# Kernel optimization log

Measured on AMD Instinct MI355X. Metric: run time of the kernel, lower is better.

## Reference

```python
import jax, jax.numpy as jnp
import numpy as np

N_NODES = 50000
N_EDGES = 625000
D = 128
H = 128

def setup_inputs() -> dict:
    key = jax.random.key(0)
    ks = jax.random.split(key, 6)
    z = jax.random.normal(ks[0], (N_NODES, D), dtype=jnp.float32)
    edge_index = jax.random.randint(ks[1], (2, N_EDGES), 0, N_NODES, dtype=jnp.int64)
    # MLP params (Linear stores y = x @ W + b here; W is [in, out])
    W1 = jax.random.normal(ks[2], (2 * D, H), dtype=jnp.float32) * (1.0 / np.sqrt(2 * D))
    b1 = jnp.zeros((H,), dtype=jnp.float32)
    W2 = jax.random.normal(ks[3], (H, H // 2), dtype=jnp.float32) * (1.0 / np.sqrt(H))
    b2 = jnp.zeros((H // 2,), dtype=jnp.float32)
    W3 = jax.random.normal(ks[4], (H // 2, 1), dtype=jnp.float32) * (1.0 / np.sqrt(H // 2))
    b3 = jnp.zeros((1,), dtype=jnp.float32)
    return {"z": z, "edge_index": edge_index, "W1": W1, "b1": b1,
            "W2": W2, "b2": b2, "W3": W3, "b3": b3}

def reference(z, edge_index, W1, b1, W2, b2, W3, b3):
    # Gather edge endpoints: z_i [E, D], z_j [E, D]
    z_i = z[edge_index[0]]
    z_j = z[edge_index[1]]
    edge_feat = jnp.concatenate([z_i, z_j], axis=-1)  # [E, 2D]
    h = jax.nn.relu(edge_feat @ W1 + b1)              # [E, H]  (dropout = identity, eval)
    h = jax.nn.relu(h @ W2 + b2)                      # [E, H//2]
    scores = (h @ W3 + b3)[:, 0]                      # [E]
    return scores
```

## Files before the change

kernel.cpp:

```cpp
#include <hip/hip_runtime.h>

#define NEDGE 625000
#define NNODE 50000
#define WPITCH 136
#define EPITCH 68

typedef __bf16 bf16x8 __attribute__((ext_vector_type(8)));
typedef unsigned short u16x8 __attribute__((ext_vector_type(8)));
typedef float f32x4 __attribute__((ext_vector_type(4)));

__device__ __forceinline__ unsigned short f32_bf16(float f) {
  __bf16 h = (__bf16)f;
  return __builtin_bit_cast(unsigned short, h);
}
__device__ __forceinline__ float bf16_f32(unsigned short h) {
  return (float)__builtin_bit_cast(__bf16, h);
}

__global__ __launch_bounds__(256) void prep_kernel(
    const float* __restrict__ W1, const float* __restrict__ W2,
    const int* __restrict__ ei,
    unsigned short* __restrict__ WcatT, unsigned short* __restrict__ W2T,
    int* __restrict__ idx64_flag)
{
  int i = blockIdx.x * 256 + threadIdx.x;
  if (i < 256 * 128) {
    int jp = i >> 7, k = i & 127;
    float v = (jp < 128) ? W1[k * 128 + jp] : W1[(128 + k) * 128 + (jp - 128)];
    WcatT[jp * 128 + k] = f32_bf16(v);
  } else if (i < 256 * 128 + 64 * 128) {
    int i2 = i - 256 * 128;
    int n = i2 >> 7, k = i2 & 127;
    W2T[n * 128 + k] = f32_bf16(W2[k * 64 + n]);
  }
  if (i == 0) {
    int allz = 1;
    for (int j = 1; j < 64; j += 2) allz &= (ei[j] == 0);
    *idx64_flag = allz;
  }
}

__global__ __launch_bounds__(64) void uv_kernel(
    const float* __restrict__ z, const float* __restrict__ b1,
    const unsigned short* __restrict__ WcatT,
    unsigned short* __restrict__ UV)
{
  __shared__ unsigned short st[16 * EPITCH];
  const int lane = threadIdx.x & 63, c = lane & 15, q = lane >> 4;
  const int mbase = blockIdx.x * 16;
  const int rA = mbase + c;
  const int rAc = (rA < NNODE) ? rA : 0;

  bf16x8 a0[4];
  {
    const float* zA = z + (size_t)rAc * 128 + q * 8;
    float4 fA[4][2];
#pragma unroll
    for (int kt = 0; kt < 4; ++kt) {
      fA[kt][0] = ((const float4*)(zA + kt * 32))[0];
      fA[kt][1] = ((const float4*)(zA + kt * 32))[1];
    }
#pragma unroll
    for (int kt = 0; kt < 4; ++kt) {
      const float* pa = (const float*)&fA[kt][0];
      bf16x8 oa;
#pragma unroll
      for (int j = 0; j < 8; ++j) oa[j] = (__bf16)pa[j];
      a0[kt] = oa;
    }
  }

  for (int nc = 0; nc < 4; ++nc) {
    f32x4 acc[4];
#pragma unroll
    for (int nt = 0; nt < 4; ++nt) {
      f32x4 zz = {0.f, 0.f, 0.f, 0.f};
      acc[nt] = zz;
    }

#pragma unroll
    for (int kt = 0; kt < 4; ++kt) {
#pragma unroll
      for (int nt = 0; nt < 4; ++nt) {
        bf16x8 bb = *(const bf16x8*)(WcatT + (size_t)(nc * 64 + nt * 16 + c) * 128 + kt * 32 + q * 8);
        acc[nt] = __builtin_amdgcn_mfma_f32_16x16x32_bf16(a0[kt], bb, acc[nt], 0, 0, 0);
      }
    }

    float badd[4];
#pragma unroll
    for (int nt = 0; nt < 4; ++nt) {
      int col = nc * 64 + nt * 16 + c;
      badd[nt] = (col < 128) ? b1[col] : 0.f;
    }

#pragma unroll
    for (int nt = 0; nt < 4; ++nt)
#pragma unroll
      for (int reg = 0; reg < 4; ++reg)
        st[(q * 4 + reg) * EPITCH + nt * 16 + c] = f32_bf16(acc[nt][reg] + badd[nt]);
    __asm__ volatile("s_waitcnt lgkmcnt(0)" ::: "memory");

    {
      int lrow = lane >> 2, qt = lane & 3;
      int grow = mbase + lrow;
      u16x8 d0 = *(u16x8*)&st[lrow * EPITCH + qt * 16 + 0];
      u16x8 d1 = *(u16x8*)&st[lrow * EPITCH + qt * 16 + 8];
      if (grow < NNODE) {
        u16x8* dst = (u16x8*)(UV + (size_t)grow * 256 + nc * 64 + qt * 16);
        dst[0] = d0;
        dst[1] = d1;
      }
    }
    __asm__ volatile("s_waitcnt lgkmcnt(0)" ::: "memory");
  }
}

__global__ __launch_bounds__(256, 4) void edge_kernel(
    const int* __restrict__ ei,
    const unsigned short* __restrict__ UV,
    const unsigned short* __restrict__ W2T,
    const float* __restrict__ b2, const float* __restrict__ W3,
    const float* __restrict__ b3, const int* __restrict__ idx64_flag,
    float* __restrict__ out)
{
  __shared__ unsigned short lW[64 * WPITCH];
  const int t = threadIdx.x, wave = t >> 6, lane = t & 63, c = lane & 15, q = lane >> 4;

  {
    int n = t >> 2, qd = t & 3;
    const u16x8* src = (const u16x8*)(W2T + n * 128 + qd * 32);
    u16x8* dst = (u16x8*)(&lW[n * WPITCH + qd * 32]);
#pragma unroll
    for (int i = 0; i < 4; ++i) dst[i] = src[i];
  }
  __syncthreads();

  const int ebase = blockIdx.x * 128 + wave * 32;
  const int eA = ebase + c, eB = ebase + 16 + c;
  const int eAc = (eA < NEDGE) ? eA : 0;
  const int eBc = (eB < NEDGE) ? eB : 0;
  int sA, dA, sB, dB;
  if (*idx64_flag) {
    const long long* e64 = (const long long*)ei;
    sA = (int)e64[eAc]; dA = (int)e64[NEDGE + eAc];
    sB = (int)e64[eBc]; dB = (int)e64[NEDGE + eBc];
  } else {
    sA = ei[eAc]; dA = ei[NEDGE + eAc];
    sB = ei[eBc]; dB = ei[NEDGE + eBc];
  }

  const u16x8* pAu = (const u16x8*)(UV + (size_t)sA * 256) + q;
  const u16x8* pAv = (const u16x8*)(UV + (size_t)dA * 256 + 128) + q;
  const u16x8* pBu = (const u16x8*)(UV + (size_t)sB * 256) + q;
  const u16x8* pBv = (const u16x8*)(UV + (size_t)dB * 256 + 128) + q;
  u16x8 rAu[4], rAv[4], rBu[4], rBv[4];
#pragma unroll
  for (int kt = 0; kt < 4; ++kt) {
    rAu[kt] = pAu[kt * 4];
    rAv[kt] = pAv[kt * 4];
    rBu[kt] = pBu[kt * 4];
    rBv[kt] = pBv[kt * 4];
  }

  f32x4 acc[2][4];
#pragma unroll
  for (int mt = 0; mt < 2; ++mt)
#pragma unroll
    for (int nt = 0; nt < 4; ++nt) {
      f32x4 zz = {0.f, 0.f, 0.f, 0.f};
      acc[mt][nt] = zz;
    }

#pragma unroll
  for (int kt = 0; kt < 4; ++kt) {
    bf16x8 a0, a1;
#pragma unroll
    for (int j = 0; j < 8; ++j) {
      a0[j] = (__bf16)fmaxf(bf16_f32(rAu[kt][j]) + bf16_f32(rAv[kt][j]), 0.f);
      a1[j] = (__bf16)fmaxf(bf16_f32(rBu[kt][j]) + bf16_f32(rBv[kt][j]), 0.f);
    }
#pragma unroll
    for (int nt = 0; nt < 4; ++nt) {
      bf16x8 bb = *(const bf16x8*)(&lW[(nt * 16 + c) * WPITCH + kt * 32 + q * 8]);
      acc[0][nt] = __builtin_amdgcn_mfma_f32_16x16x32_bf16(a0, bb, acc[0][nt], 0, 0, 0);
      acc[1][nt] = __builtin_amdgcn_mfma_f32_16x16x32_bf16(a1, bb, acc[1][nt], 0, 0, 0);
    }
  }

  float b2v[4], w3v[4];
#pragma unroll
  for (int nt = 0; nt < 4; ++nt) {
    int n = nt * 16 + c;
    b2v[nt] = b2[n];
    w3v[nt] = W3[n];
  }
  float bias3 = b3[0];

#pragma unroll
  for (int mt = 0; mt < 2; ++mt) {
    float p0 = 0.f, p1 = 0.f, p2 = 0.f, p3 = 0.f;
#pragma unroll
    for (int nt = 0; nt < 4; ++nt) {
      p0 += fmaxf(acc[mt][nt][0] + b2v[nt], 0.f) * w3v[nt];
      p1 += fmaxf(acc[mt][nt][1] + b2v[nt], 0.f) * w3v[nt];
      p2 += fmaxf(acc[mt][nt][2] + b2v[nt], 0.f) * w3v[nt];
      p3 += fmaxf(acc[mt][nt][3] + b2v[nt], 0.f) * w3v[nt];
    }
#pragma unroll
    for (int m = 1; m < 16; m <<= 1) {
      p0 += __shfl_xor(p0, m, 64);
      p1 += __shfl_xor(p1, m, 64);
      p2 += __shfl_xor(p2, m, 64);
      p3 += __shfl_xor(p3, m, 64);
    }
    if (c == 0) {
      int eb = ebase + mt * 16 + q * 4;
      if (eb + 0 < NEDGE) out[eb + 0] = p0 + bias3;
      if (eb + 1 < NEDGE) out[eb + 1] = p1 + bias3;
      if (eb + 2 < NEDGE) out[eb + 2] = p2 + bias3;
      if (eb + 3 < NEDGE) out[eb + 3] = p3 + bias3;
    }
  }
}

extern "C" void kernel_launch(void* const* d_in, const int* in_sizes, int n_in,
                              void* d_out, int out_size, void* d_ws, size_t ws_size,
                              hipStream_t stream) {
  const float* z  = (const float*)d_in[0];
  const int*   ei = (const int*)d_in[1];
  const float* W1 = (const float*)d_in[2];
  const float* b1 = (const float*)d_in[3];
  const float* W2 = (const float*)d_in[4];
  const float* b2 = (const float*)d_in[5];
  const float* W3 = (const float*)d_in[6];
  const float* b3 = (const float*)d_in[7];
  float* out = (float*)d_out;

  unsigned short* UV    = (unsigned short*)d_ws;
  unsigned short* WcatT = UV + (size_t)NNODE * 256;
  unsigned short* W2T   = WcatT + 256 * 128;
  int* idx64_flag       = (int*)(W2T + 64 * 128);

  prep_kernel<<<dim3(160), dim3(256), 0, stream>>>(W1, W2, ei, WcatT, W2T, idx64_flag);
  uv_kernel<<<dim3((NNODE + 15) / 16), dim3(64), 0, stream>>>(z, b1, WcatT, UV);
  edge_kernel<<<dim3((NEDGE + 127) / 128), dim3(256), 0, stream>>>(
      ei, UV, W2T, b2, W3, b3, idx64_flag, out);
}
```

Baseline: 156.8 us.

## Fuse prep, node projection and edge MLP into one cooperative persistent kernel

Replaces three separate launches with a single cooperative kernel that uses grid-wide syncs between the weight-prep, per-node UV projection and per-edge MLP phases. Each phase becomes a grid-stride loop over a persistent grid sized from occupancy queries. This removes launch gaps and kernel tail effects, and lets each block load W2 into LDS once instead of once per edge tile. In exchange it adds two grid barriers and constrains the edge phase to a smaller persistent grid, which may reduce latency hiding for the random gathers.

```diff
diff --git a/kernel.cpp b/kernel.cpp
--- a/kernel.cpp
+++ b/kernel.cpp
@@ -1,9 +1,14 @@
 #include <hip/hip_runtime.h>
+#include <hip/hip_cooperative_groups.h>
+
+namespace cg = cooperative_groups;
 
 #define NEDGE 625000
 #define NNODE 50000
 #define WPITCH 136
 #define EPITCH 68
+#define NTILE ((NEDGE + 127) / 128)
+#define NUNIT ((NNODE + 15) / 16)
 
 typedef __bf16 bf16x8 __attribute__((ext_vector_type(8)));
 typedef unsigned short u16x8 __attribute__((ext_vector_type(8)));
@@ -17,209 +22,208 @@
   return (float)__builtin_bit_cast(__bf16, h);
 }
 
-__global__ __launch_bounds__(256) void prep_kernel(
-    const float* __restrict__ W1, const float* __restrict__ W2,
-    const int* __restrict__ ei,
-    unsigned short* __restrict__ WcatT, unsigned short* __restrict__ W2T,
-    int* __restrict__ idx64_flag)
+__global__ __launch_bounds__(256, 4) void fused_kernel(
+    const float* __restrict__ z, const int* ei,
+    const float* __restrict__ W1, const float* __restrict__ b1,
+    const float* __restrict__ W2, const float* __restrict__ b2,
+    const float* __restrict__ W3, const float* __restrict__ b3,
+    unsigned short* UV, unsigned short* WcatT, unsigned short* W2T,
+    int* idx64_flag, float* __restrict__ out)
 {
-  int i = blockIdx.x * 256 + threadIdx.x;
-  if (i < 256 * 128) {
-    int jp = i >> 7, k = i & 127;
-    float v = (jp < 128) ? W1[k * 128 + jp] : W1[(128 + k) * 128 + (jp - 128)];
-    WcatT[jp * 128 + k] = f32_bf16(v);
-  } else if (i < 256 * 128 + 64 * 128) {
-    int i2 = i - 256 * 128;
-    int n = i2 >> 7, k = i2 & 127;
-    W2T[n * 128 + k] = f32_bf16(W2[k * 64 + n]);
-  }
-  if (i == 0) {
-    int allz = 1;
-    for (int j = 1; j < 64; j += 2) allz &= (ei[j] == 0);
-    *idx64_flag = allz;
-  }
-}
-
-__global__ __launch_bounds__(64) void uv_kernel(
-    const float* __restrict__ z, const float* __restrict__ b1,
-    const unsigned short* __restrict__ WcatT,
-    unsigned short* __restrict__ UV)
-{
-  __shared__ unsigned short st[16 * EPITCH];
-  const int lane = threadIdx.x & 63, c = lane & 15, q = lane >> 4;
-  const int mbase = blockIdx.x * 16;
-  const int rA = mbase + c;
-  const int rAc = (rA < NNODE) ? rA : 0;
-
-  bf16x8 a0[4];
+  __shared__ unsigned short lds[64 * WPITCH];
+  cg::grid_group grid = cg::this_grid();
+  const int t = threadIdx.x, wave = t >> 6, lane = t & 63, c = lane & 15, q = lane >> 4;
+  const int bid = blockIdx.x;
+  const int nblk = gridDim.x;
+
+  for (int i = bid * 256 + t; i < 256 * 128 + 64 * 128; i += nblk * 256) {
+    if (i < 256 * 128) {
+      int jp = i >> 7, k = i & 127;
+      float v = (jp < 128) ? W1[k * 128 + jp] : W1[(128 + k) * 128 + (jp - 128)];
+      WcatT[jp * 128 + k] = f32_bf16(v);
+    } else {
+      int i2 = i - 256 * 128;
+      int n = i2 >> 7, k = i2 & 127;
+      W2T[n * 128 + k] = f32_bf16(W2[k * 64 + n]);
+    }
+  }
+  if (bid == 0 && t < 64) {
+    int v = ei[t];
+    unsigned long long odd_nz = __ballot((t & 1) && v != 0);
+    if (t == 0) *idx64_flag = (odd_nz == 0ull) ? 1 : 0;
+  }
+  __threadfence();
+  grid.sync();
+
   {
-    const float* zA = z + (size_t)rAc * 128 + q * 8;
-    float4 fA[4][2];
-#pragma unroll
-    for (int kt = 0; kt < 4; ++kt) {
-      fA[kt][0] = ((const float4*)(zA + kt * 32))[0];
-      fA[kt][1] = ((const float4*)(zA + kt * 32))[1];
-    }
-#pragma unroll
-    for (int kt = 0; kt < 4; ++kt) {
-      const float* pa = (const float*)&fA[kt][0];
-      bf16x8 oa;
-#pragma unroll
-      for (int j = 0; j < 8; ++j) oa[j] = (__bf16)pa[j];
-      a0[kt] = oa;
-    }
-  }
-
-  for (int nc = 0; nc < 4; ++nc) {
-    f32x4 acc[4];
-#pragma unroll
-    for (int nt = 0; nt < 4; ++nt) {
-      f32x4 zz = {0.f, 0.f, 0.f, 0.f};
-      acc[nt] = zz;
-    }
-
-#pragma unroll
-    for (int kt = 0; kt < 4; ++kt) {
-#pragma unroll
-      for (int nt = 0; nt < 4; ++nt) {
-        bf16x8 bb = *(const bf16x8*)(WcatT + (size_t)(nc * 64 + nt * 16 + c) * 128 + kt * 32 + q * 8);
-        acc[nt] = __builtin_amdgcn_mfma_f32_16x16x32_bf16(a0[kt], bb, acc[nt], 0, 0, 0);
-      }
-    }
-
-    float badd[4];
-#pragma unroll
-    for (int nt = 0; nt < 4; ++nt) {
-      int col = nc * 64 + nt * 16 + c;
-      badd[nt] = (col < 128) ? b1[col] : 0.f;
-    }
-
-#pragma unroll
-    for (int nt = 0; nt < 4; ++nt)
-#pragma unroll
-      for (int reg = 0; reg < 4; ++reg)
-        st[(q * 4 + reg) * EPITCH + nt * 16 + c] = f32_bf16(acc[nt][reg] + badd[nt]);
-    __asm__ volatile("s_waitcnt lgkmcnt(0)" ::: "memory");
-
-    {
-      int lrow = lane >> 2, qt = lane & 3;
-      int grow = mbase + lrow;
-      u16x8 d0 = *(u16x8*)&st[lrow * EPITCH + qt * 16 + 0];
-      u16x8 d1 = *(u16x8*)&st[lrow * EPITCH + qt * 16 + 8];
-      if (grow < NNODE) {
-        u16x8* dst = (u16x8*)(UV + (size_t)grow * 256 + nc * 64 + qt * 16);
-        dst[0] = d0;
-        dst[1] = d1;
-      }
-    }
-    __asm__ volatile("s_waitcnt lgkmcnt(0)" ::: "memory");
-  }
-}
-
-__global__ __launch_bounds__(256, 4) void edge_kernel(
-    const int* __restrict__ ei,
-    const unsigned short* __restrict__ UV,
-    const unsigned short* __restrict__ W2T,
-    const float* __restrict__ b2, const float* __restrict__ W3,
-    const float* __restrict__ b3, const int* __restrict__ idx64_flag,
-    float* __restrict__ out)
-{
-  __shared__ unsigned short lW[64 * WPITCH];
-  const int t = threadIdx.x, wave = t >> 6, lane = t & 63, c = lane & 15, q = lane >> 4;
+    unsigned short* my = &lds[wave * 16 * EPITCH];
+    const int gw0 = bid * 4 + wave, gstride = nblk * 4;
+    for (int gw = gw0; gw < NUNIT; gw += gstride) {
+      const int mbase = gw * 16;
+      const int rA = mbase + c;
+      const int rAc = (rA < NNODE) ? rA : 0;
+
+      bf16x8 a0[4];
+      {
+        const float* zA = z + (size_t)rAc * 128 + q * 8;
+        float4 fA[4][2];
+#pragma unroll
+        for (int kt = 0; kt < 4; ++kt) {
+          fA[kt][0] = ((const float4*)(zA + kt * 32))[0];
+          fA[kt][1] = ((const float4*)(zA + kt * 32))[1];
+        }
+#pragma unroll
+        for (int kt = 0; kt < 4; ++kt) {
+          const float* pa = (const float*)&fA[kt][0];
+          bf16x8 oa;
+#pragma unroll
+          for (int j = 0; j < 8; ++j) oa[j] = (__bf16)pa[j];
+          a0[kt] = oa;
+        }
+      }
+
+      for (int nc = 0; nc < 4; ++nc) {
+        f32x4 acc[4];
+#pragma unroll
+        for (int nt = 0; nt < 4; ++nt) {
+          f32x4 zz = {0.f, 0.f, 0.f, 0.f};
+          acc[nt] = zz;
+        }
+#pragma unroll
+        for (int kt = 0; kt < 4; ++kt) {
+#pragma unroll
+          for (int nt = 0; nt < 4; ++nt) {
+            bf16x8 bb = *(const bf16x8*)(WcatT + (size_t)(nc * 64 + nt * 16 + c) * 128 + kt * 32 + q * 8);
+            acc[nt] = __builtin_amdgcn_mfma_f32_16x16x32_bf16(a0[kt], bb, acc[nt], 0, 0, 0);
+          }
+        }
+        float badd[4];
+#pragma unroll
+        for (int nt = 0; nt < 4; ++nt) {
+          int col = nc * 64 + nt * 16 + c;
+          badd[nt] = (col < 128) ? b1[col] : 0.f;
+        }
+#pragma unroll
+        for (int nt = 0; nt < 4; ++nt)
+#pragma unroll
+          for (int reg = 0; reg < 4; ++reg)
+            my[(q * 4 + reg) * EPITCH + nt * 16 + c] = f32_bf16(acc[nt][reg] + badd[nt]);
+        __asm__ volatile("s_waitcnt lgkmcnt(0)" ::: "memory");
+
+        {
+          int lrow = lane >> 2, qt = lane & 3;
+          int grow = mbase + lrow;
+          u16x8 d0 = *(u16x8*)&my[lrow * EPITCH + qt * 16 + 0];
+          u16x8 d1 = *(u16x8*)&my[lrow * EPITCH + qt * 16 + 8];
+          if (grow < NNODE) {
+            u16x8* dst = (u16x8*)(UV + (size_t)grow * 256 + nc * 64 + qt * 16);
+            dst[0] = d0;
+            dst[1] = d1;
+          }
+        }
+        __asm__ volatile("s_waitcnt lgkmcnt(0)" ::: "memory");
+      }
+    }
+  }
+  __threadfence();
+  grid.sync();
 
   {
     int n = t >> 2, qd = t & 3;
     const u16x8* src = (const u16x8*)(W2T + n * 128 + qd * 32);
-    u16x8* dst = (u16x8*)(&lW[n * WPITCH + qd * 32]);
+    u16x8* dst = (u16x8*)(&lds[n * WPITCH + qd * 32]);
 #pragma unroll
     for (int i = 0; i < 4; ++i) dst[i] = src[i];
   }
   __syncthreads();
-
-  const int ebase = blockIdx.x * 128 + wave * 32;
-  const int eA = ebase + c, eB = ebase + 16 + c;
-  const int eAc = (eA < NEDGE) ? eA : 0;
-  const int eBc = (eB < NEDGE) ? eB : 0;
-  int sA, dA, sB, dB;
-  if (*idx64_flag) {
-    const long long* e64 = (const long long*)ei;
-    sA = (int)e64[eAc]; dA = (int)e64[NEDGE + eAc];
-    sB = (int)e64[eBc]; dB = (int)e64[NEDGE + eBc];
-  } else {
-    sA = ei[eAc]; dA = ei[NEDGE + eAc];
-    sB = ei[eBc]; dB = ei[NEDGE + eBc];
-  }
-
-  const u16x8* pAu = (const u16x8*)(UV + (size_t)sA * 256) + q;
-  const u16x8* pAv = (const u16x8*)(UV + (size_t)dA * 256 + 128) + q;
-  const u16x8* pBu = (const u16x8*)(UV + (size_t)sB * 256) + q;
-  const u16x8* pBv = (const u16x8*)(UV + (size_t)dB * 256 + 128) + q;
-  u16x8 rAu[4], rAv[4], rBu[4], rBv[4];
-#pragma unroll
-  for (int kt = 0; kt < 4; ++kt) {
-    rAu[kt] = pAu[kt * 4];
-    rAv[kt] = pAv[kt * 4];
-    rBu[kt] = pBu[kt * 4];
-    rBv[kt] = pBv[kt * 4];
-  }
-
-  f32x4 acc[2][4];
-#pragma unroll
-  for (int mt = 0; mt < 2; ++mt)
+  const int i64 = *idx64_flag;
+
+  for (int tile = bid; tile < NTILE; tile += nblk) {
+    const int ebase = tile * 128 + wave * 32;
+    const int eA = ebase + c, eB = ebase + 16 + c;
+    const int eAc = (eA < NEDGE) ? eA : 0;
+    const int eBc = (eB < NEDGE) ? eB : 0;
+    int sA, dA, sB, dB;
+    if (i64) {
+      const long long* e64 = (const long long*)ei;
+      sA = (int)e64[eAc]; dA = (int)e64[NEDGE + eAc];
+      sB = (int)e64[eBc]; dB = (int)e64[NEDGE + eBc];
+    } else {
+      sA = ei[eAc]; dA = ei[NEDGE + eAc];
+      sB = ei[eBc]; dB = ei[NEDGE + eBc];
+    }
+
+    const u16x8* pAu = (const u16x8*)(UV + (size_t)sA * 256) + q;
+    const u16x8* pAv = (const u16x8*)(UV + (size_t)dA * 256 + 128) + q;
+    const u16x8* pBu = (const u16x8*)(UV + (size_t)sB * 256) + q;
+    const u16x8* pBv = (const u16x8*)(UV + (size_t)dB * 256 + 128) + q;
+    u16x8 rAu[4], rAv[4], rBu[4], rBv[4];
+#pragma unroll
+    for (int kt = 0; kt < 4; ++kt) {
+      rAu[kt] = pAu[kt * 4];
+      rAv[kt] = pAv[kt * 4];
+      rBu[kt] = pBu[kt * 4];
+      rBv[kt] = pBv[kt * 4];
+    }
+
+    f32x4 acc[2][4];
+#pragma unroll
+    for (int mt = 0; mt < 2; ++mt)
+#pragma unroll
+      for (int nt = 0; nt < 4; ++nt) {
+        f32x4 zz = {0.f, 0.f, 0.f, 0.f};
+        acc[mt][nt] = zz;
+      }
+
+#pragma unroll
+    for (int kt = 0; kt < 4; ++kt) {
+      bf16x8 a0, a1;
+#pragma unroll
+      for (int j = 0; j < 8; ++j) {
+        a0[j] = (__bf16)fmaxf(bf16_f32(rAu[kt][j]) + bf16_f32(rAv[kt][j]), 0.f);
+        a1[j] = (__bf16)fmaxf(bf16_f32(rBu[kt][j]) + bf16_f32(rBv[kt][j]), 0.f);
+      }
+#pragma unroll
+      for (int nt = 0; nt < 4; ++nt) {
+        bf16x8 bb = *(const bf16x8*)(&lds[(nt * 16 + c) * WPITCH + kt * 32 + q * 8]);
+        acc[0][nt] = __builtin_amdgcn_mfma_f32_16x16x32_bf16(a0, bb, acc[0][nt], 0, 0, 0);
+        acc[1][nt] = __builtin_amdgcn_mfma_f32_16x16x32_bf16(a1, bb, acc[1][nt], 0, 0, 0);
+      }
+    }
+
+    float b2v[4], w3v[4];
 #pragma unroll
     for (int nt = 0; nt < 4; ++nt) {
-      f32x4 zz = {0.f, 0.f, 0.f, 0.f};
-      acc[mt][nt] = zz;
-    }
-
-#pragma unroll
-  for (int kt = 0; kt < 4; ++kt) {
-    bf16x8 a0, a1;
-#pragma unroll
-    for (int j = 0; j < 8; ++j) {
-      a0[j] = (__bf16)fmaxf(bf16_f32(rAu[kt][j]) + bf16_f32(rAv[kt][j]), 0.f);
-      a1[j] = (__bf16)fmaxf(bf16_f32(rBu[kt][j]) + bf16_f32(rBv[kt][j]), 0.f);
-    }
-#pragma unroll
-    for (int nt = 0; nt < 4; ++nt) {
-      bf16x8 bb = *(const bf16x8*)(&lW[(nt * 16 + c) * WPITCH + kt * 32 + q * 8]);
-      acc[0][nt] = __builtin_amdgcn_mfma_f32_16x16x32_bf16(a0, bb, acc[0][nt], 0, 0, 0);
-      acc[1][nt] = __builtin_amdgcn_mfma_f32_16x16x32_bf16(a1, bb, acc[1][nt], 0, 0, 0);
-    }
-  }
-
-  float b2v[4], w3v[4];
-#pragma unroll
-  for (int nt = 0; nt < 4; ++nt) {
-    int n = nt * 16 + c;
-    b2v[nt] = b2[n];
-    w3v[nt] = W3[n];
-  }
-  float bias3 = b3[0];
-
-#pragma unroll
-  for (int mt = 0; mt < 2; ++mt) {
-    float p0 = 0.f, p1 = 0.f, p2 = 0.f, p3 = 0.f;
-#pragma unroll
-    for (int nt = 0; nt < 4; ++nt) {
-      p0 += fmaxf(acc[mt][nt][0] + b2v[nt], 0.f) * w3v[nt];
-      p1 += fmaxf(acc[mt][nt][1] + b2v[nt], 0.f) * w3v[nt];
-      p2 += fmaxf(acc[mt][nt][2] + b2v[nt], 0.f) * w3v[nt];
-      p3 += fmaxf(acc[mt][nt][3] + b2v[nt], 0.f) * w3v[nt];
-    }
-#pragma unroll
-    for (int m = 1; m < 16; m <<= 1) {
-      p0 += __shfl_xor(p0, m, 64);
-      p1 += __shfl_xor(p1, m, 64);
-      p2 += __shfl_xor(p2, m, 64);
-      p3 += __shfl_xor(p3, m, 64);
-    }
-    if (c == 0) {
-      int eb = ebase + mt * 16 + q * 4;
-      if (eb + 0 < NEDGE) out[eb + 0] = p0 + bias3;
-      if (eb + 1 < NEDGE) out[eb + 1] = p1 + bias3;
-      if (eb + 2 < NEDGE) out[eb + 2] = p2 + bias3;
-      if (eb + 3 < NEDGE) out[eb + 3] = p3 + bias3;
+      int n = nt * 16 + c;
+      b2v[nt] = b2[n];
+      w3v[nt] = W3[n];
+    }
+    float bias3 = b3[0];
+
+#pragma unroll
+    for (int mt = 0; mt < 2; ++mt) {
+      float p0 = 0.f, p1 = 0.f, p2 = 0.f, p3 = 0.f;
+#pragma unroll
+      for (int nt = 0; nt < 4; ++nt) {
+        p0 += fmaxf(acc[mt][nt][0] + b2v[nt], 0.f) * w3v[nt];
+        p1 += fmaxf(acc[mt][nt][1] + b2v[nt], 0.f) * w3v[nt];
+        p2 += fmaxf(acc[mt][nt][2] + b2v[nt], 0.f) * w3v[nt];
+        p3 += fmaxf(acc[mt][nt][3] + b2v[nt], 0.f) * w3v[nt];
+      }
+#pragma unroll
+      for (int m = 1; m < 16; m <<= 1) {
+        p0 += __shfl_xor(p0, m, 64);
+        p1 += __shfl_xor(p1, m, 64);
+        p2 += __shfl_xor(p2, m, 64);
+        p3 += __shfl_xor(p3, m, 64);
+      }
+      if (c == 0) {
+        int eb = ebase + mt * 16 + q * 4;
+        if (eb + 0 < NEDGE) out[eb + 0] = p0 + bias3;
+        if (eb + 1 < NEDGE) out[eb + 1] = p1 + bias3;
+        if (eb + 2 < NEDGE) out[eb + 2] = p2 + bias3;
+        if (eb + 3 < NEDGE) out[eb + 3] = p3 + bias3;
+      }
     }
   }
 }
@@ -242,8 +246,25 @@
   unsigned short* W2T   = WcatT + 256 * 128;
   int* idx64_flag       = (int*)(W2T + 64 * 128);
 
-  prep_kernel<<<dim3(160), dim3(256), 0, stream>>>(W1, W2, ei, WcatT, W2T, idx64_flag);
-  uv_kernel<<<dim3((NNODE + 15) / 16), dim3(64), 0, stream>>>(z, b1, WcatT, UV);
-  edge_kernel<<<dim3((NEDGE + 127) / 128), dim3(256), 0, stream>>>(
-      ei, UV, W2T, b2, W3, b3, idx64_flag, out);
-}
+  static int coopGrid = 0;
+  if (coopGrid == 0) {
+    int perCU = 0;
+    if (hipOccupancyMaxActiveBlocksPerMultiprocessor(&perCU, fused_kernel, 256, 0) != hipSuccess ||
+        perCU <= 0)
+      perCU = 3;
+    int nCU = 256;
+    hipDeviceProp_t prop;
+    int dev = 0;
+    if (hipGetDevice(&dev) == hipSuccess && hipGetDeviceProperties(&prop, dev) == hipSuccess)
+      nCU = prop.multiProcessorCount;
+    coopGrid = perCU * nCU;
+    if (coopGrid > 2048) coopGrid = 2048;
+    if (coopGrid < 256) coopGrid = 256;
+  }
+
+  void* args[] = {(void*)&z,  (void*)&ei, (void*)&W1, (void*)&b1, (void*)&W2,
+                  (void*)&b2, (void*)&W3, (void*)&b3, (void*)&UV, (void*)&WcatT,
+                  (void*)&W2T, (void*)&idx64_flag, (void*)&out};
+  hipLaunchCooperativeKernel((const void*)fused_kernel, dim3(coopGrid), dim3(256), args, 0,
+                             stream);
+}
```

Result: slower. 464.9 us (+196.6%).

## Fuse weight prep into uv kernel and stage transposed W1 in LDS

Applied to the files above, without the earlier changes.

Removes the separate prep kernel launch by having the uv kernel convert and transpose W1 into shared memory per block, while two blocks also build W2T and the index-width flag. The uv kernel now uses 256-thread blocks covering 64 nodes, with B operands read from LDS instead of global memory. The cost is that every block redundantly converts all of W1 (32K elements) and needs about 70KB of LDS, which limits occupancy.

```diff
diff --git a/kernel.cpp b/kernel.cpp
--- a/kernel.cpp
+++ b/kernel.cpp
@@ -4,6 +4,7 @@
 #define NNODE 50000
 #define WPITCH 136
 #define EPITCH 68
+#define WCPITCH 136
 
 typedef __bf16 bf16x8 __attribute__((ext_vector_type(8)));
 typedef unsigned short u16x8 __attribute__((ext_vector_type(8)));
@@ -17,37 +18,40 @@
   return (float)__builtin_bit_cast(__bf16, h);
 }
 
-__global__ __launch_bounds__(256) void prep_kernel(
-    const float* __restrict__ W1, const float* __restrict__ W2,
+__global__ __launch_bounds__(256, 2) void uv_kernel(
+    const float* __restrict__ z, const float* __restrict__ W1,
+    const float* __restrict__ b1, const float* __restrict__ W2,
     const int* __restrict__ ei,
-    unsigned short* __restrict__ WcatT, unsigned short* __restrict__ W2T,
+    unsigned short* __restrict__ UV, unsigned short* __restrict__ W2T,
     int* __restrict__ idx64_flag)
 {
-  int i = blockIdx.x * 256 + threadIdx.x;
-  if (i < 256 * 128) {
-    int jp = i >> 7, k = i & 127;
-    float v = (jp < 128) ? W1[k * 128 + jp] : W1[(128 + k) * 128 + (jp - 128)];
-    WcatT[jp * 128 + k] = f32_bf16(v);
-  } else if (i < 256 * 128 + 64 * 128) {
-    int i2 = i - 256 * 128;
-    int n = i2 >> 7, k = i2 & 127;
-    W2T[n * 128 + k] = f32_bf16(W2[k * 64 + n]);
-  }
-  if (i == 0) {
+  __shared__ unsigned short lWc[256 * WCPITCH];
+  __shared__ unsigned short st[4 * 16 * EPITCH];
+  const int t = threadIdx.x, wave = t >> 6, lane = t & 63, c = lane & 15, q = lane >> 4;
+  const int bid = blockIdx.x;
+
+  if (bid < 2) {
+    for (int e = bid * 4096 + t; e < (bid + 1) * 4096; e += 256) {
+      int n = e >> 7, k = e & 127;
+      W2T[n * 128 + k] = f32_bf16(W2[k * 64 + n]);
+    }
+  }
+  if (bid == 0 && t == 0) {
     int allz = 1;
     for (int j = 1; j < 64; j += 2) allz &= (ei[j] == 0);
     *idx64_flag = allz;
   }
-}
-
-__global__ __launch_bounds__(64) void uv_kernel(
-    const float* __restrict__ z, const float* __restrict__ b1,
-    const unsigned short* __restrict__ WcatT,
-    unsigned short* __restrict__ UV)
-{
-  __shared__ unsigned short st[16 * EPITCH];
-  const int lane = threadIdx.x & 63, c = lane & 15, q = lane >> 4;
-  const int mbase = blockIdx.x * 16;
+
+  for (int e = t; e < 256 * 128; e += 256) {
+    int r = e >> 7, j = e & 127;
+    float v = W1[r * 128 + j];
+    int jp = (r < 128) ? j : (128 + j);
+    int k = r & 127;
+    lWc[jp * WCPITCH + k] = f32_bf16(v);
+  }
+  __syncthreads();
+
+  const int mbase = bid * 64 + wave * 16;
   const int rA = mbase + c;
   const int rAc = (rA < NNODE) ? rA : 0;
 
@@ -70,6 +74,8 @@
     }
   }
 
+  unsigned short* my = &st[wave * 16 * EPITCH];
+
   for (int nc = 0; nc < 4; ++nc) {
     f32x4 acc[4];
 #pragma unroll
@@ -77,15 +83,13 @@
       f32x4 zz = {0.f, 0.f, 0.f, 0.f};
       acc[nt] = zz;
     }
-
-#pragma unroll
-    for (int kt = 0; kt < 4; ++kt) {
+#pragma unroll
+    for (int kt = 0; kt < 4; ++kt)
 #pragma unroll
       for (int nt = 0; nt < 4; ++nt) {
-        bf16x8 bb = *(const bf16x8*)(WcatT + (size_t)(nc * 64 + nt * 16 + c) * 128 + kt * 32 + q * 8);
+        bf16x8 bb = *(const bf16x8*)(&lWc[(nc * 64 + nt * 16 + c) * WCPITCH + kt * 32 + q * 8]);
         acc[nt] = __builtin_amdgcn_mfma_f32_16x16x32_bf16(a0[kt], bb, acc[nt], 0, 0, 0);
       }
-    }
 
     float badd[4];
 #pragma unroll
@@ -98,14 +102,14 @@
     for (int nt = 0; nt < 4; ++nt)
 #pragma unroll
       for (int reg = 0; reg < 4; ++reg)
-        st[(q * 4 + reg) * EPITCH + nt * 16 + c] = f32_bf16(acc[nt][reg] + badd[nt]);
+        my[(q * 4 + reg) * EPITCH + nt * 16 + c] = f32_bf16(acc[nt][reg] + badd[nt]);
     __asm__ volatile("s_waitcnt lgkmcnt(0)" ::: "memory");
 
     {
       int lrow = lane >> 2, qt = lane & 3;
       int grow = mbase + lrow;
-      u16x8 d0 = *(u16x8*)&st[lrow * EPITCH + qt * 16 + 0];
-      u16x8 d1 = *(u16x8*)&st[lrow * EPITCH + qt * 16 + 8];
+      u16x8 d0 = *(u16x8*)&my[lrow * EPITCH + qt * 16 + 0];
+      u16x8 d1 = *(u16x8*)&my[lrow * EPITCH + qt * 16 + 8];
       if (grow < NNODE) {
         u16x8* dst = (u16x8*)(UV + (size_t)grow * 256 + nc * 64 + qt * 16);
         dst[0] = d0;
@@ -237,13 +241,12 @@
   const float* b3 = (const float*)d_in[7];
   float* out = (float*)d_out;
 
-  unsigned short* UV    = (unsigned short*)d_ws;
-  unsigned short* WcatT = UV + (size_t)NNODE * 256;
-  unsigned short* W2T   = WcatT + 256 * 128;
-  int* idx64_flag       = (int*)(W2T + 64 * 128);
-
-  prep_kernel<<<dim3(160), dim3(256), 0, stream>>>(W1, W2, ei, WcatT, W2T, idx64_flag);
-  uv_kernel<<<dim3((NNODE + 15) / 16), dim3(64), 0, stream>>>(z, b1, WcatT, UV);
+  unsigned short* UV  = (unsigned short*)d_ws;
+  unsigned short* W2T = UV + (size_t)NNODE * 256;
+  int* idx64_flag     = (int*)(W2T + 64 * 128);
+
+  uv_kernel<<<dim3((NNODE + 63) / 64), dim3(256), 0, stream>>>(
+      z, W1, b1, W2, ei, UV, W2T, idx64_flag);
   edge_kernel<<<dim3((NEDGE + 127) / 128), dim3(256), 0, stream>>>(
       ei, UV, W2T, b2, W3, b3, idx64_flag, out);
 }
```

Result: faster. 152.5 us (median of 2 runs) (-2.7%).
